# Kernel tuning notes

Measured on AMD Instinct MI355X. Metric: run time of the kernel, lower is better.

Reference implementation:

```python
import jax, jax.numpy as jnp
import numpy as np

N_NODES = 50000
N_EDGES = 800000


def _norm(deg):
    # DGL: norm = deg^-0.5 with inf (zero-degree) replaced by 0
    return jnp.where(deg > 0, jax.lax.rsqrt(jnp.maximum(deg, 1.0)), 0.0)


def setup_inputs() -> dict:
    key = jax.random.key(0)
    ks = jax.random.split(key, 8)
    x = jax.random.normal(ks[0], (N_NODES, 128), dtype=jnp.float32)
    W1 = jax.random.normal(ks[1], (128, 128), dtype=jnp.float32) * (1.0 / np.sqrt(128))
    b1 = jnp.zeros((128,), dtype=jnp.float32)
    W2 = jax.random.normal(ks[2], (128, 8), dtype=jnp.float32) * (1.0 / np.sqrt(128))
    b2 = jnp.zeros((8,), dtype=jnp.float32)
    src = jax.random.randint(ks[3], (N_EDGES,), 0, N_NODES, dtype=jnp.int32)
    dst = jax.random.randint(ks[4], (N_EDGES,), 0, N_NODES, dtype=jnp.int32)
    graph_ids = jnp.sort(jax.random.randint(ks[5], (N_NODES,), 0, 100, dtype=jnp.int32))
    return {"x": x, "W1": W1, "b1": b1, "W2": W2, "b2": b2,
            "src": src, "dst": dst, "graph_ids": graph_ids, "num_graphs": 100}


def _graph_conv(x, W, b, src, dst, norm_src, norm_dst):
    # GraphConv norm='both': out = D_in^{-1/2} A (D_out^{-1/2} x W) + b
    h = x @ W                                   # [N, F_out]
    msg = h[src] * norm_src[src, None]          # gather + src norm, [E, F_out]
    agg = jax.ops.segment_sum(msg, dst, num_segments=x.shape[0])  # scatter-add
    return agg * norm_dst[:, None] + b


def reference(x, W1, b1, W2, b2, src, dst, graph_ids, num_graphs):
    n = x.shape[0]
    ones_e = jnp.ones((src.shape[0],), dtype=x.dtype)
    deg_out = jax.ops.segment_sum(ones_e, src, num_segments=n)
    deg_in = jax.ops.segment_sum(ones_e, dst, num_segments=n)
    norm_src = _norm(deg_out)
    norm_dst = _norm(deg_in)

    h = _graph_conv(x, W1, b1, src, dst, norm_src, norm_dst)
    h = jax.nn.relu(h)
    h = _graph_conv(h, W2, b2, src, dst, norm_src, norm_dst)

    # dgl.mean_nodes: per-graph mean of node features
    counts = jax.ops.segment_sum(jnp.ones((n,), dtype=x.dtype), graph_ids,
                                 num_segments=num_graphs)
    sums = jax.ops.segment_sum(h, graph_ids, num_segments=num_graphs)
    return sums / jnp.maximum(counts, 1.0)[:, None]
```

## Files before the change

### kernel.cpp

```cpp
#include <hip/hip_runtime.h>

#define F1 128
#define F2 8
#define CAP 64
#define RH 8192
#define ECH 16384
#define BK 32

typedef unsigned short us8 __attribute__((ext_vector_type(8)));

__device__ inline unsigned short f2bf(float f) {
  unsigned u = __float_as_uint(f);
  u += 0x7FFF + ((u >> 16) & 1);
  return (unsigned short)(u >> 16);
}
__device__ inline float bf2f(unsigned short h) {
  return __uint_as_float(((unsigned)h) << 16);
}

__global__ __launch_bounds__(256) void k_hist(const int* __restrict__ src,
                                              const int* __restrict__ dst,
                                              unsigned short* __restrict__ src16,
                                              unsigned short* __restrict__ dst16,
                                              int* __restrict__ partialA,
                                              int* __restrict__ partialB,
                                              int Epad, int E, int N) {
  __shared__ int binsA[RH];
  __shared__ int binsB[RH];
  int range0 = blockIdx.x * RH;
  int c = blockIdx.y;
  int t = threadIdx.x;
  bool writer = (blockIdx.x == 0);
  for (int i = t; i < RH; i += 256) { binsA[i] = 0; binsB[i] = 0; }
  __syncthreads();
  int e0 = c * ECH, e1 = min(e0 + ECH, Epad);
  for (int base = e0 + t * 4; base < e1; base += 1024) {
    int4 a, b;
    if (base + 4 <= E) {
      a = *(const int4*)&src[base];
      b = *(const int4*)&dst[base];
    } else {
      a.x = (base + 0 < E) ? src[base + 0] : -1;
      a.y = (base + 1 < E) ? src[base + 1] : -1;
      a.z = (base + 2 < E) ? src[base + 2] : -1;
      a.w = (base + 3 < E) ? src[base + 3] : -1;
      b.x = (base + 0 < E) ? dst[base + 0] : -1;
      b.y = (base + 1 < E) ? dst[base + 1] : -1;
      b.z = (base + 2 < E) ? dst[base + 2] : -1;
      b.w = (base + 3 < E) ? dst[base + 3] : -1;
    }
    int av[4] = {a.x, a.y, a.z, a.w};
    int bv[4] = {b.x, b.y, b.z, b.w};
#pragma unroll
    for (int j = 0; j < 4; ++j) {
      int sn = av[j] - range0;
      if (av[j] >= 0 && (unsigned)sn < (unsigned)RH) atomicAdd(&binsA[sn], 1);
      int dn = bv[j] - range0;
      if (bv[j] >= 0 && (unsigned)dn < (unsigned)RH) atomicAdd(&binsB[dn], 1);
    }
    if (writer) {
      ushort4 sa, sb;
      sa.x = av[0] >= 0 ? (unsigned short)av[0] : 0xFFFF;
      sa.y = av[1] >= 0 ? (unsigned short)av[1] : 0xFFFF;
      sa.z = av[2] >= 0 ? (unsigned short)av[2] : 0xFFFF;
      sa.w = av[3] >= 0 ? (unsigned short)av[3] : 0xFFFF;
      sb.x = bv[0] >= 0 ? (unsigned short)bv[0] : 0xFFFF;
      sb.y = bv[1] >= 0 ? (unsigned short)bv[1] : 0xFFFF;
      sb.z = bv[2] >= 0 ? (unsigned short)bv[2] : 0xFFFF;
      sb.w = bv[3] >= 0 ? (unsigned short)bv[3] : 0xFFFF;
      *(ushort4*)&src16[base] = sa;
      *(ushort4*)&dst16[base] = sb;
    }
  }
  __syncthreads();
  for (int i = t; i < RH; i += 256) {
    int n = range0 + i;
    if (n < N) {
      partialA[c * N + n] = binsA[i];
      partialB[c * N + n] = binsB[i];
    }
  }
}

__global__ void k_starts(const int* __restrict__ partialA, const int* __restrict__ partialB,
                         int* __restrict__ starts, int* __restrict__ cnt,
                         float* __restrict__ norm_src, float* __restrict__ norm_dst,
                         unsigned short* __restrict__ esrc16,
                         unsigned short* __restrict__ h1n,
                         float* __restrict__ h2n,
                         float* __restrict__ gsum,
                         int* __restrict__ done,
                         const int* __restrict__ gids,
                         float* __restrict__ rcnt,
                         int N, int NCH, int NG) {
  int n = blockIdx.x * 256 + threadIdx.x;
  if (n == 0) *done = 0;
  if (n < NG * F2) gsum[n] = 0.f;
  if (n < NG) {
    int g = n;
    int lo = 0, hi = N;
    while (lo < hi) { int m = (lo + hi) >> 1; if (gids[m] < g) lo = m + 1; else hi = m; }
    int lb = lo;
    lo = 0; hi = N;
    while (lo < hi) { int m = (lo + hi) >> 1; if (gids[m] <= g) lo = m + 1; else hi = m; }
    rcnt[g] = 1.f / fmaxf((float)(lo - lb), 1.f);
  }
  if (n < 16) {
    us8 z = {0, 0, 0, 0, 0, 0, 0, 0};
    *(us8*)&h1n[(size_t)N * 128 + n * 8] = z;
  }
  if (n < 8) h2n[(size_t)N * 8 + n] = 0.f;
  if (n < N) {
    int dout = 0;
#pragma unroll 8
    for (int c = 0; c < NCH; ++c) dout += partialA[c * N + n];
    int run = n * CAP;
#pragma unroll 8
    for (int c = 0; c < NCH; ++c) {
      starts[c * N + n] = run;
      run += partialB[c * N + n];
    }
    int din = run - n * CAP;
    int cn = min(din, CAP);
    cnt[n] = cn;
    int cp = (cn + 15) & ~15;
    for (int pos = cn; pos < cp; ++pos) esrc16[n * CAP + pos] = (unsigned short)N;
    norm_src[n] = dout > 0 ? rsqrtf((float)dout) : 0.f;
    norm_dst[n] = din > 0 ? rsqrtf((float)din) : 0.f;
  }
}

struct SMemU {
  union {
    int cur[RH];
    struct { float xsT[BK][132]; float Wl[BK][132]; } g;
  } u;
};

__global__ __launch_bounds__(256) void k_scatgemm(const unsigned short* __restrict__ src16,
                                                  const unsigned short* __restrict__ dst16,
                                                  const int* __restrict__ starts,
                                                  unsigned short* __restrict__ esrc16,
                                                  const float* __restrict__ x,
                                                  const float* __restrict__ W1,
                                                  const float* __restrict__ norm_src,
                                                  unsigned short* __restrict__ h1n,
                                                  int Epad, int N, int NCH, int NRNCH) {
  __shared__ SMemU sm;
  int tid = threadIdx.x;
  if ((int)blockIdx.x < NRNCH) {
    int range0 = ((int)blockIdx.x / NCH) * RH;
    int c = (int)blockIdx.x % NCH;
    for (int i = tid; i < RH; i += 256) {
      int n = range0 + i;
      sm.u.cur[i] = (n < N) ? starts[c * N + n] : 0;
    }
    __syncthreads();
    int e0 = c * ECH, e1 = min(e0 + ECH, Epad);
    for (int base = e0 + tid * 8; base < e1; base += 2048) {
      us8 a = *(const us8*)&src16[base];
      us8 b = *(const us8*)&dst16[base];
#pragma unroll
      for (int j = 0; j < 8; ++j) {
        int dn = (int)b[j] - range0;
        if ((unsigned)dn < (unsigned)RH) {
          int node = range0 + dn;
          int p = atomicAdd(&sm.u.cur[dn], 1);
          if (p < (node + 1) * CAP) esrc16[p] = a[j];
        }
      }
    }
  } else {
    int row0 = ((int)blockIdx.x - NRNCH) * 128;
    int tc = tid & 15;
    int tr = tid >> 4;
    float acc[8][8] = {{0.f}};
    for (int kb = 0; kb < 128; kb += BK) {
      __syncthreads();
#pragma unroll
      for (int it = 0; it < 4; ++it) {
        int i = tid + it * 256;
        int r = i >> 3, kq = i & 7;
        int grow = row0 + r;
        float4 v = make_float4(0.f, 0.f, 0.f, 0.f);
        if (grow < N) v = *(const float4*)&x[(size_t)grow * 128 + kb + kq * 4];
        sm.u.g.xsT[kq * 4 + 0][r] = v.x;
        sm.u.g.xsT[kq * 4 + 1][r] = v.y;
        sm.u.g.xsT[kq * 4 + 2][r] = v.z;
        sm.u.g.xsT[kq * 4 + 3][r] = v.w;
      }
#pragma unroll
      for (int it = 0; it < 4; ++it) {
        int i = tid + it * 256;
        int k = i >> 5, c4 = i & 31;
        *(float4*)&sm.u.g.Wl[k][c4 * 4] = *(const float4*)&W1[(size_t)(kb + k) * 128 + c4 * 4];
      }
      __syncthreads();
#pragma unroll 2
      for (int k = 0; k < BK; ++k) {
        float4 xa = *(float4*)&sm.u.g.xsT[k][tr * 8];
        float4 xb = *(float4*)&sm.u.g.xsT[k][tr * 8 + 4];
        float4 wa = *(float4*)&sm.u.g.Wl[k][tc * 8];
        float4 wb = *(float4*)&sm.u.g.Wl[k][tc * 8 + 4];
        float xs[8] = {xa.x, xa.y, xa.z, xa.w, xb.x, xb.y, xb.z, xb.w};
        float ws[8] = {wa.x, wa.y, wa.z, wa.w, wb.x, wb.y, wb.z, wb.w};
#pragma unroll
        for (int i = 0; i < 8; ++i)
#pragma unroll
          for (int j = 0; j < 8; ++j) acc[i][j] += xs[i] * ws[j];
      }
    }
#pragma unroll
    for (int i = 0; i < 8; ++i) {
      int grow = row0 + tr * 8 + i;
      if (grow < N) {
        float ns = norm_src[grow];
        us8 o;
#pragma unroll
        for (int j = 0; j < 8; ++j) o[j] = f2bf(acc[i][j] * ns);
        *(us8*)&h1n[(size_t)grow * 128 + tc * 8] = o;
      }
    }
  }
}

__global__ __launch_bounds__(256) void k_agg1f(const unsigned short* __restrict__ h1n,
                                               const int* __restrict__ cnt,
                                               const unsigned short* __restrict__ esrc16,
                                               const float* __restrict__ norm_dst,
                                               const float* __restrict__ norm_src,
                                               const float* __restrict__ b1,
                                               const float* __restrict__ W2,
                                               float* __restrict__ h2n, int N) {
  int tid = threadIdx.x;
  int lane = tid & 63;
  int g = lane >> 4;
  int fl = lane & 15;
  int node = (blockIdx.x * 256 + tid - lane) / 16 + g;
  if (node >= N) return;
  int cp = (cnt[node] + 15) & ~15;
  int i0 = node * CAP;
  float acc[8] = {0.f, 0.f, 0.f, 0.f, 0.f, 0.f, 0.f, 0.f};
  for (int i = 0; i < cp; i += 16) {
#pragma unroll
    for (int t4 = 0; t4 < 16; t4 += 4) {
      ushort4 ss = *(const ushort4*)&esrc16[i0 + i + t4];
      us8 v0 = *(const us8*)&h1n[(size_t)ss.x * 128 + fl * 8];
      us8 v1 = *(const us8*)&h1n[(size_t)ss.y * 128 + fl * 8];
      us8 v2 = *(const us8*)&h1n[(size_t)ss.z * 128 + fl * 8];
      us8 v3 = *(const us8*)&h1n[(size_t)ss.w * 128 + fl * 8];
#pragma unroll
      for (int j = 0; j < 8; ++j)
        acc[j] += (bf2f(v0[j]) + bf2f(v1[j])) + (bf2f(v2[j]) + bf2f(v3[j]));
    }
  }
  float nd = norm_dst[node];
  float4 bb0 = *(const float4*)&b1[fl * 8];
  float4 bb1 = *(const float4*)&b1[fl * 8 + 4];
  float r[8];
  r[0] = fmaxf(acc[0] * nd + bb0.x, 0.f);
  r[1] = fmaxf(acc[1] * nd + bb0.y, 0.f);
  r[2] = fmaxf(acc[2] * nd + bb0.z, 0.f);
  r[3] = fmaxf(acc[3] * nd + bb0.w, 0.f);
  r[4] = fmaxf(acc[4] * nd + bb1.x, 0.f);
  r[5] = fmaxf(acc[5] * nd + bb1.y, 0.f);
  r[6] = fmaxf(acc[6] * nd + bb1.z, 0.f);
  r[7] = fmaxf(acc[7] * nd + bb1.w, 0.f);
  float4 pa = make_float4(0.f, 0.f, 0.f, 0.f);
  float4 pb = make_float4(0.f, 0.f, 0.f, 0.f);
#pragma unroll
  for (int jj = 0; jj < 8; ++jj) {
    float4 wa = *(const float4*)&W2[(fl * 8 + jj) * 8];
    float4 wb = *(const float4*)&W2[(fl * 8 + jj) * 8 + 4];
    pa.x += r[jj] * wa.x; pa.y += r[jj] * wa.y;
    pa.z += r[jj] * wa.z; pa.w += r[jj] * wa.w;
    pb.x += r[jj] * wb.x; pb.y += r[jj] * wb.y;
    pb.z += r[jj] * wb.z; pb.w += r[jj] * wb.w;
  }
#pragma unroll
  for (int d = 8; d >= 1; d >>= 1) {
    pa.x += __shfl_down(pa.x, d); pa.y += __shfl_down(pa.y, d);
    pa.z += __shfl_down(pa.z, d); pa.w += __shfl_down(pa.w, d);
    pb.x += __shfl_down(pb.x, d); pb.y += __shfl_down(pb.y, d);
    pb.z += __shfl_down(pb.z, d); pb.w += __shfl_down(pb.w, d);
  }
  if (fl == 0) {
    float ns = norm_src[node];
    pa.x *= ns; pa.y *= ns; pa.z *= ns; pa.w *= ns;
    pb.x *= ns; pb.y *= ns; pb.z *= ns; pb.w *= ns;
    *(float4*)&h2n[(size_t)node * 8] = pa;
    *(float4*)&h2n[(size_t)node * 8 + 4] = pb;
  }
}

__global__ __launch_bounds__(256) void k_agg2pool(const float* __restrict__ h2n,
                                                  const int* __restrict__ cnt,
                                                  const unsigned short* __restrict__ esrc16,
                                                  const float* __restrict__ norm_dst,
                                                  const float* __restrict__ b2,
                                                  const int* __restrict__ gids,
                                                  float* __restrict__ gsum,
                                                  float* __restrict__ out,
                                                  int* __restrict__ done,
                                                  const float* __restrict__ rcnt,
                                                  int NG, int N) {
  __shared__ float bins[16 * 8];
  __shared__ int sg0;
  __shared__ bool last;
  int tid = threadIdx.x;
  if (tid < 128) bins[tid] = 0.f;
  int base = blockIdx.x * 32;
  if (tid == 0) sg0 = gids[min(base, N - 1)];
  __syncthreads();
  int node = base + (tid >> 3);
  int j = tid & 7;
  if (node < N) {
    int cp = (cnt[node] + 15) & ~15;
    int i0 = node * CAP;
    float acc = 0.f;
    for (int i = 0; i < cp; i += 8) {
      us8 ss = *(const us8*)&esrc16[i0 + i];
      acc += ((h2n[(size_t)ss[0] * 8 + j] + h2n[(size_t)ss[1] * 8 + j]) +
              (h2n[(size_t)ss[2] * 8 + j] + h2n[(size_t)ss[3] * 8 + j])) +
             ((h2n[(size_t)ss[4] * 8 + j] + h2n[(size_t)ss[5] * 8 + j]) +
              (h2n[(size_t)ss[6] * 8 + j] + h2n[(size_t)ss[7] * 8 + j]));
    }
    float r = acc * norm_dst[node] + b2[j];
    int delta = gids[node] - sg0;
    if (delta < 16) atomicAdd(&bins[delta * 8 + j], r);
    else atomicAdd(&gsum[gids[node] * 8 + j], r);
  }
  __syncthreads();
  if (tid < 128) {
    float v = bins[tid];
    if (v != 0.f) atomicAdd(&gsum[(sg0 + (tid >> 3)) * 8 + (tid & 7)], v);
  }
  __syncthreads();
  if (tid == 0) {
    __threadfence();
    last = (atomicAdd(done, 1) == (int)gridDim.x - 1);
  }
  __syncthreads();
  if (last) {
    __threadfence();
    for (int i = tid; i < NG * F2; i += 256) {
      float gv = atomicAdd(&gsum[i], 0.f);
      out[i] = gv * rcnt[i >> 3];
    }
  }
}

extern "C" void kernel_launch(void* const* d_in, const int* in_sizes, int n_in,
                              void* d_out, int out_size, void* d_ws, size_t ws_size,
                              hipStream_t stream) {
  const float* x  = (const float*)d_in[0];
  const float* W1 = (const float*)d_in[1];
  const float* b1 = (const float*)d_in[2];
  const float* W2 = (const float*)d_in[3];
  const float* b2 = (const float*)d_in[4];
  const int* src  = (const int*)d_in[5];
  const int* dst  = (const int*)d_in[6];
  const int* gids = (const int*)d_in[7];
  int N = in_sizes[0] / F1;
  int E = in_sizes[5];
  int NG = out_size / F2;
  float* out = (float*)d_out;

  int Epad = (E + 2047) & ~2047;
  int NR  = (N + RH - 1) / RH;
  int NCH = (Epad + ECH - 1) / ECH;
  int NRNCH = NR * NCH;
  int gemmB = (N + 127) / 128;

  char* p = (char*)d_ws;
  auto alloc = [&](size_t bytes) -> void* {
    void* r = (void*)p;
    p += (bytes + 255) & ~(size_t)255;
    return r;
  };
  float* gsum    = (float*)alloc((size_t)NG * F2 * 4);
  int* done      = (int*)alloc(256);
  float* rcnt    = (float*)alloc((size_t)NG * 4);
  unsigned short* src16 = (unsigned short*)alloc((size_t)Epad * 2);
  unsigned short* dst16 = (unsigned short*)alloc((size_t)Epad * 2);
  int* cnt       = (int*)alloc((size_t)N * 4);
  float* norm_src = (float*)alloc((size_t)N * 4);
  float* norm_dst = (float*)alloc((size_t)N * 4);
  unsigned short* esrc16 = (unsigned short*)alloc((size_t)N * CAP * 2);
  unsigned short* h1n = (unsigned short*)alloc((size_t)(N + 1) * F1 * 2);
  float* h2n     = (float*)alloc((size_t)(N + 1) * F2 * 4);
  int* partialA  = (int*)alloc((size_t)NCH * N * 4);
  int* partialB  = (int*)alloc((size_t)NCH * N * 4);
  int* starts    = (int*)alloc((size_t)NCH * N * 4);
  (void)ws_size; (void)n_in;

  k_hist<<<dim3(NR, NCH), 256, 0, stream>>>(src, dst, src16, dst16,
                                            partialA, partialB, Epad, E, N);
  k_starts<<<(N + 255) / 256, 256, 0, stream>>>(partialA, partialB, starts, cnt,
                                                norm_src, norm_dst, esrc16, h1n, h2n,
                                                gsum, done, gids, rcnt, N, NCH, NG);
  k_scatgemm<<<NRNCH + gemmB, 256, 0, stream>>>(src16, dst16, starts, esrc16,
                                                x, W1, norm_src, h1n, Epad, N, NCH, NRNCH);
  k_agg1f<<<(N + 15) / 16, 256, 0, stream>>>(h1n, cnt, esrc16, norm_dst, norm_src, b1, W2, h2n, N);
  k_agg2pool<<<((N * 8 + 255) / 256), 256, 0, stream>>>(h2n, cnt, esrc16, norm_dst, b2,
                                                        gids, gsum, out, done, rcnt, NG, N);
}
```

Baseline: 250.0 us.

## Split fused scatter/GEMM kernel into separate launches and remap GEMM column tiles

Splits the combined scatter+GEMM kernel into two launches, a CSR scatter kernel and a dedicated first-layer GEMM kernel. Each now gets its own shared memory sizing and register allocation instead of the union. The GEMM also changes each thread's column mapping from 8 contiguous columns to two groups of 4 separated by 64, meant to cut LDS bank conflicts on W reads, and it writes output as two ushort4 stores. The split adds a launch and removes the overlap the single kernel had between scatter and GEMM blocks.

```diff
diff --git a/kernel.cpp b/kernel.cpp
--- a/kernel.cpp
+++ b/kernel.cpp
@@ -130,96 +130,95 @@
   }
 }
 
-struct SMemU {
-  union {
-    int cur[RH];
-    struct { float xsT[BK][132]; float Wl[BK][132]; } g;
-  } u;
-};
-
-__global__ __launch_bounds__(256) void k_scatgemm(const unsigned short* __restrict__ src16,
-                                                  const unsigned short* __restrict__ dst16,
-                                                  const int* __restrict__ starts,
-                                                  unsigned short* __restrict__ esrc16,
-                                                  const float* __restrict__ x,
-                                                  const float* __restrict__ W1,
-                                                  const float* __restrict__ norm_src,
-                                                  unsigned short* __restrict__ h1n,
-                                                  int Epad, int N, int NCH, int NRNCH) {
-  __shared__ SMemU sm;
+__global__ __launch_bounds__(256) void k_scatter(const unsigned short* __restrict__ src16,
+                                                 const unsigned short* __restrict__ dst16,
+                                                 const int* __restrict__ starts,
+                                                 unsigned short* __restrict__ esrc16,
+                                                 int Epad, int N, int NCH) {
+  __shared__ int cur[RH];
+  int range0 = ((int)blockIdx.x / NCH) * RH;
+  int c = (int)blockIdx.x % NCH;
+  int t = threadIdx.x;
+  for (int i = t; i < RH; i += 256) {
+    int n = range0 + i;
+    cur[i] = (n < N) ? starts[c * N + n] : 0;
+  }
+  __syncthreads();
+  int e0 = c * ECH, e1 = min(e0 + ECH, Epad);
+  for (int base = e0 + t * 8; base < e1; base += 2048) {
+    us8 a = *(const us8*)&src16[base];
+    us8 b = *(const us8*)&dst16[base];
+#pragma unroll
+    for (int j = 0; j < 8; ++j) {
+      int dn = (int)b[j] - range0;
+      if ((unsigned)dn < (unsigned)RH) {
+        int node = range0 + dn;
+        int p = atomicAdd(&cur[dn], 1);
+        if (p < (node + 1) * CAP) esrc16[p] = a[j];
+      }
+    }
+  }
+}
+
+__global__ __launch_bounds__(256) void k_gemm1(const float* __restrict__ x,
+                                               const float* __restrict__ W1,
+                                               const float* __restrict__ norm_src,
+                                               unsigned short* __restrict__ h1n, int N) {
+  __shared__ float xsT[BK][132];
+  __shared__ float Wl[BK][132];
+  int row0 = blockIdx.x * 128;
   int tid = threadIdx.x;
-  if ((int)blockIdx.x < NRNCH) {
-    int range0 = ((int)blockIdx.x / NCH) * RH;
-    int c = (int)blockIdx.x % NCH;
-    for (int i = tid; i < RH; i += 256) {
-      int n = range0 + i;
-      sm.u.cur[i] = (n < N) ? starts[c * N + n] : 0;
-    }
+  int tc = tid & 15;
+  int tr = tid >> 4;
+  float acc[8][8] = {{0.f}};
+
+  for (int kb = 0; kb < 128; kb += BK) {
     __syncthreads();
-    int e0 = c * ECH, e1 = min(e0 + ECH, Epad);
-    for (int base = e0 + tid * 8; base < e1; base += 2048) {
-      us8 a = *(const us8*)&src16[base];
-      us8 b = *(const us8*)&dst16[base];
-#pragma unroll
-      for (int j = 0; j < 8; ++j) {
-        int dn = (int)b[j] - range0;
-        if ((unsigned)dn < (unsigned)RH) {
-          int node = range0 + dn;
-          int p = atomicAdd(&sm.u.cur[dn], 1);
-          if (p < (node + 1) * CAP) esrc16[p] = a[j];
-        }
-      }
-    }
-  } else {
-    int row0 = ((int)blockIdx.x - NRNCH) * 128;
-    int tc = tid & 15;
-    int tr = tid >> 4;
-    float acc[8][8] = {{0.f}};
-    for (int kb = 0; kb < 128; kb += BK) {
-      __syncthreads();
-#pragma unroll
-      for (int it = 0; it < 4; ++it) {
-        int i = tid + it * 256;
-        int r = i >> 3, kq = i & 7;
-        int grow = row0 + r;
-        float4 v = make_float4(0.f, 0.f, 0.f, 0.f);
-        if (grow < N) v = *(const float4*)&x[(size_t)grow * 128 + kb + kq * 4];
-        sm.u.g.xsT[kq * 4 + 0][r] = v.x;
-        sm.u.g.xsT[kq * 4 + 1][r] = v.y;
-        sm.u.g.xsT[kq * 4 + 2][r] = v.z;
-        sm.u.g.xsT[kq * 4 + 3][r] = v.w;
-      }
-#pragma unroll
-      for (int it = 0; it < 4; ++it) {
-        int i = tid + it * 256;
-        int k = i >> 5, c4 = i & 31;
-        *(float4*)&sm.u.g.Wl[k][c4 * 4] = *(const float4*)&W1[(size_t)(kb + k) * 128 + c4 * 4];
-      }
-      __syncthreads();
+#pragma unroll
+    for (int it = 0; it < 4; ++it) {
+      int i = tid + it * 256;
+      int r = i >> 3, kq = i & 7;
+      int grow = row0 + r;
+      float4 v = make_float4(0.f, 0.f, 0.f, 0.f);
+      if (grow < N) v = *(const float4*)&x[(size_t)grow * 128 + kb + kq * 4];
+      xsT[kq * 4 + 0][r] = v.x;
+      xsT[kq * 4 + 1][r] = v.y;
+      xsT[kq * 4 + 2][r] = v.z;
+      xsT[kq * 4 + 3][r] = v.w;
+    }
+#pragma unroll
+    for (int it = 0; it < 4; ++it) {
+      int i = tid + it * 256;
+      int k = i >> 5, c4 = i & 31;
+      *(float4*)&Wl[k][c4 * 4] = *(const float4*)&W1[(size_t)(kb + k) * 128 + c4 * 4];
+    }
+    __syncthreads();
 #pragma unroll 2
-      for (int k = 0; k < BK; ++k) {
-        float4 xa = *(float4*)&sm.u.g.xsT[k][tr * 8];
-        float4 xb = *(float4*)&sm.u.g.xsT[k][tr * 8 + 4];
-        float4 wa = *(float4*)&sm.u.g.Wl[k][tc * 8];
-        float4 wb = *(float4*)&sm.u.g.Wl[k][tc * 8 + 4];
-        float xs[8] = {xa.x, xa.y, xa.z, xa.w, xb.x, xb.y, xb.z, xb.w};
-        float ws[8] = {wa.x, wa.y, wa.z, wa.w, wb.x, wb.y, wb.z, wb.w};
-#pragma unroll
-        for (int i = 0; i < 8; ++i)
-#pragma unroll
-          for (int j = 0; j < 8; ++j) acc[i][j] += xs[i] * ws[j];
-      }
-    }
-#pragma unroll
-    for (int i = 0; i < 8; ++i) {
-      int grow = row0 + tr * 8 + i;
-      if (grow < N) {
-        float ns = norm_src[grow];
-        us8 o;
-#pragma unroll
-        for (int j = 0; j < 8; ++j) o[j] = f2bf(acc[i][j] * ns);
-        *(us8*)&h1n[(size_t)grow * 128 + tc * 8] = o;
-      }
+    for (int k = 0; k < BK; ++k) {
+      float4 xa = *(float4*)&xsT[k][tr * 8];
+      float4 xb = *(float4*)&xsT[k][tr * 8 + 4];
+      float4 wa = *(float4*)&Wl[k][tc * 4];
+      float4 wb = *(float4*)&Wl[k][tc * 4 + 64];
+      float xs[8] = {xa.x, xa.y, xa.z, xa.w, xb.x, xb.y, xb.z, xb.w};
+      float ws[8] = {wa.x, wa.y, wa.z, wa.w, wb.x, wb.y, wb.z, wb.w};
+#pragma unroll
+      for (int i = 0; i < 8; ++i)
+#pragma unroll
+        for (int j = 0; j < 8; ++j) acc[i][j] += xs[i] * ws[j];
+    }
+  }
+#pragma unroll
+  for (int i = 0; i < 8; ++i) {
+    int grow = row0 + tr * 8 + i;
+    if (grow < N) {
+      float ns = norm_src[grow];
+      ushort4 oa, ob;
+      oa.x = f2bf(acc[i][0] * ns); oa.y = f2bf(acc[i][1] * ns);
+      oa.z = f2bf(acc[i][2] * ns); oa.w = f2bf(acc[i][3] * ns);
+      ob.x = f2bf(acc[i][4] * ns); ob.y = f2bf(acc[i][5] * ns);
+      ob.z = f2bf(acc[i][6] * ns); ob.w = f2bf(acc[i][7] * ns);
+      *(ushort4*)&h1n[(size_t)grow * 128 + tc * 4] = oa;
+      *(ushort4*)&h1n[(size_t)grow * 128 + 64 + tc * 4] = ob;
     }
   }
 }
@@ -369,8 +368,6 @@
   int Epad = (E + 2047) & ~2047;
   int NR  = (N + RH - 1) / RH;
   int NCH = (Epad + ECH - 1) / ECH;
-  int NRNCH = NR * NCH;
-  int gemmB = (N + 127) / 128;
 
   char* p = (char*)d_ws;
   auto alloc = [&](size_t bytes) -> void* {
@@ -399,8 +396,8 @@
   k_starts<<<(N + 255) / 256, 256, 0, stream>>>(partialA, partialB, starts, cnt,
                                                 norm_src, norm_dst, esrc16, h1n, h2n,
                                                 gsum, done, gids, rcnt, N, NCH, NG);
-  k_scatgemm<<<NRNCH + gemmB, 256, 0, stream>>>(src16, dst16, starts, esrc16,
-                                                x, W1, norm_src, h1n, Epad, N, NCH, NRNCH);
+  k_scatter<<<NR * NCH, 256, 0, stream>>>(src16, dst16, starts, esrc16, Epad, N, NCH);
+  k_gemm1<<<(N + 127) / 128, 256, 0, stream>>>(x, W1, norm_src, h1n, N);
   k_agg1f<<<(N + 15) / 16, 256, 0, stream>>>(h1n, cnt, esrc16, norm_dst, norm_src, b1, W2, h2n, N);
   k_agg2pool<<<((N * 8 + 255) / 256), 256, 0, stream>>>(h2n, cnt, esrc16, norm_dst, b2,
                                                         gids, gsum, out, done, rcnt, NG, N);
```

Result: no change. 254.1 us (+1.7%).
